# Kernel optimization log

Measured on AMD Instinct MI355X. Metric: run time of the kernel, lower is better.

## Reference

```python
import jax, jax.numpy as jnp
import numpy as np

B, T, DIM, DIM_EPS, H = 4, 1024, 2048, 2048, 16
HD = DIM // H        # 128, value head dim
HDE = DIM_EPS // H   # 128, q/k head dim


def setup_inputs() -> dict:
    key = jax.random.key(0)
    ks = jax.random.split(key, 6)
    s = 0.02
    # rotary frequencies as in llama-style precompute (theta=10000)
    inv_freq = 1.0 / (10000.0 ** (np.arange(0, HDE, 2, dtype=np.float32) / HDE))
    t = np.arange(T, dtype=np.float32)
    ang = np.outer(t, inv_freq)  # (T, HDE//2)
    return {
        "v": jax.random.normal(ks[0], (B, T, DIM), jnp.float32),
        "x_eps": jax.random.normal(ks[1], (B, T, DIM_EPS), jnp.float32),
        "freqs_cos": jnp.asarray(np.cos(ang)),
        "freqs_sin": jnp.asarray(np.sin(ang)),
        "W_eps_attn": jax.random.normal(ks[2], (DIM_EPS, 2 * DIM_EPS), jnp.float32) * s,
        "W_attn": jax.random.normal(ks[3], (DIM, DIM), jnp.float32) * s,
        "W_proj": jax.random.normal(ks[4], (DIM, DIM), jnp.float32) * s,
        "W_eps_proj": jax.random.normal(ks[5], (DIM_EPS, DIM_EPS), jnp.float32) * s,
    }


def _rope(x, cos, sin):
    # x: (B, T, H, HDE) -> complex-multiply by freqs_cis of shape (T, HDE//2)
    xr = x.reshape(*x.shape[:-1], -1, 2)
    x_re, x_im = xr[..., 0], xr[..., 1]
    c = cos[None, :, None, :]  # (1, T, 1, HDE//2)
    s = sin[None, :, None, :]
    o_re = x_re * c - x_im * s
    o_im = x_re * s + x_im * c
    return jnp.stack([o_re, o_im], axis=-1).reshape(x.shape)


def reference(v, x_eps, freqs_cos, freqs_sin, W_eps_attn, W_attn, W_proj, W_eps_proj):
    Bn, Tn, C = v.shape
    qk = x_eps @ W_eps_attn            # (B, T, 2*DIM_EPS)
    q, k = jnp.split(qk, 2, axis=-1)
    vp = v @ W_attn                    # (B, T, DIM)
    q = _rope(q.reshape(Bn, Tn, H, HDE), freqs_cos, freqs_sin)
    k = _rope(k.reshape(Bn, Tn, H, HDE), freqs_cos, freqs_sin)
    q = q.transpose(0, 2, 1, 3)        # (B, H, T, HDE)
    k = k.transpose(0, 2, 1, 3)
    vh = vp.reshape(Bn, Tn, H, HD).transpose(0, 2, 1, 3)
    scale = 1.0 / jnp.sqrt(jnp.asarray(HDE, q.dtype))
    scores = jnp.einsum("bhqd,bhkd->bhqk", q, k) * scale
    causal = jnp.tril(jnp.ones((Tn, Tn), bool))
    scores = jnp.where(causal[None, None], scores, jnp.finfo(scores.dtype).min)
    att = jax.nn.softmax(scores, axis=-1)
    y = jnp.einsum("bhqk,bhkd->bhqd", att, vh)
    y = y.transpose(0, 2, 1, 3).reshape(Bn, Tn, C)
    v_out = y @ W_proj
    x_eps_out = x_eps @ W_eps_proj
    return (v_out, x_eps_out)
```

## Files before the change

kernel.cpp:

```cpp
#include <hip/hip_runtime.h>
#include <stdint.h>

typedef __attribute__((ext_vector_type(8))) short  short8;
typedef __attribute__((ext_vector_type(4))) float  f32x4;
typedef __attribute__((ext_vector_type(4))) float  float4v;
typedef __attribute__((ext_vector_type(4))) unsigned short ushort4v;
typedef __attribute__((ext_vector_type(4))) unsigned int   u32x4;

#define DEV __device__ __forceinline__

DEV unsigned short f2bf(float f) {
    union { float f; unsigned int u; } x; x.f = f;
    unsigned int u = x.u;
    unsigned int r = (u + 0x7fffu + ((u >> 16) & 1u)) >> 16;
    return (unsigned short)r;
}
DEV float bf2f(unsigned short b) {
    union { unsigned int u; float f; } x; x.u = ((unsigned int)b) << 16;
    return x.f;
}

DEV void gll16(const void* g, void* l) {
    __builtin_amdgcn_global_load_lds(
        (const __attribute__((address_space(1))) void*)g,
        (__attribute__((address_space(3))) void*)l, 16, 0, 0);
}

#define MROWS 4096
#define KDIM  2048
#define NQK   4096

__global__ void prep_kernel(
    const float* __restrict__ xeps, const float* __restrict__ v_in,
    const float* __restrict__ Wea, const float* __restrict__ Wa,
    const float* __restrict__ Wp,  const float* __restrict__ Wep,
    unsigned short* __restrict__ xe16, unsigned short* __restrict__ v16,
    unsigned short* __restrict__ WeaT, unsigned short* __restrict__ WaT,
    unsigned short* __restrict__ WpT,  unsigned short* __restrict__ WepT) {

    __shared__ float tile[32][33];
    const int blk = blockIdx.x, tid = threadIdx.x;

    if (blk < 16384) {
        const float* in = (blk < 8192) ? xeps : v_in;
        unsigned short* out = (blk < 8192) ? xe16 : v16;
        int i = (blk & 8191) * 256 + tid;
        float4v f = ((const float4v*)in)[i];
        ushort4v o;
        o[0] = f2bf(f[0]); o[1] = f2bf(f[1]); o[2] = f2bf(f[2]); o[3] = f2bf(f[3]);
        ((ushort4v*)out)[i] = o;
        return;
    }
    const float* W; unsigned short* Wt; int K, N, local;
    if (blk < 24576)      { W = Wea; Wt = WeaT; K = KDIM; N = NQK;  local = blk - 16384; }
    else if (blk < 28672) { W = Wa;  Wt = WaT;  K = KDIM; N = KDIM; local = blk - 24576; }
    else if (blk < 32768) { W = Wp;  Wt = WpT;  K = KDIM; N = KDIM; local = blk - 28672; }
    else                  { W = Wep; Wt = WepT; K = KDIM; N = KDIM; local = blk - 32768; }
    const int ntiles = N >> 5;
    const int n0 = (local % ntiles) * 32, k0 = (local / ntiles) * 32;
    const int tx = tid & 31, ty = tid >> 5;
#pragma unroll
    for (int j = 0; j < 32; j += 8)
        tile[ty + j][tx] = W[(size_t)(k0 + ty + j) * N + n0 + tx];
    __syncthreads();
#pragma unroll
    for (int j = 0; j < 32; j += 8)
        Wt[(size_t)(n0 + ty + j) * K + k0 + tx] = f2bf(tile[tx][ty + j]);
}

__global__ void add_f32(float* __restrict__ out, const float* __restrict__ add, int n4) {
    int i = blockIdx.x * blockDim.x + threadIdx.x;
    if (i < n4) {
        float4v a = ((const float4v*)out)[i];
        float4v b = ((const float4v*)add)[i];
        a[0] += b[0]; a[1] += b[1]; a[2] += b[2]; a[3] += b[3];
        ((float4v*)out)[i] = a;
    }
}

__global__ void transpose_v(const unsigned short* __restrict__ vp,
                            unsigned short* __restrict__ vpT) {
    __shared__ unsigned short tile[32][34];
    int tx = threadIdx.x, ty = threadIdx.y;
    int R0 = blockIdx.y * 32;
    int c0 = blockIdx.x * 32;
    int bh = R0 >> 7, d0 = R0 & 127;
    int b = bh >> 4, h = bh & 15;
#pragma unroll
    for (int j = 0; j < 32; j += 8)
        tile[ty + j][tx] = vp[(size_t)(b * 1024 + c0 + ty + j) * 2048 + h * 128 + d0 + tx];
    __syncthreads();
#pragma unroll
    for (int j = 0; j < 32; j += 8)
        vpT[(size_t)(R0 + ty + j) * 1024 + c0 + tx] = tile[tx][ty + j];
}

__global__ __launch_bounds__(512, 2) void gemm256(
    const unsigned short* __restrict__ A0g, const unsigned short* __restrict__ B0g,
    float* __restrict__ Cf0, unsigned short* __restrict__ Ch0,
    int N0, int tx0, int nb0, int outbf0,
    const unsigned short* __restrict__ A1g, const unsigned short* __restrict__ B1g,
    float* __restrict__ Cf1, unsigned short* __restrict__ Ch1,
    int N1, int tx1, int outbf1, int Kst, int Kl,
    const float* __restrict__ rC, const float* __restrict__ rS,
    int rope0, int rope1) {

    __shared__ __align__(16) char lds[131072];

    int blk = blockIdx.x;
    const unsigned short* Ag; const unsigned short* Bg;
    float* Cf; unsigned short* Ch; int N, tx, outbf, nwg, ropeF;
    if (blk < nb0) { Ag = A0g; Bg = B0g; Cf = Cf0; Ch = Ch0; N = N0; tx = tx0; outbf = outbf0; nwg = nb0; ropeF = rope0; }
    else { blk -= nb0; Ag = A1g; Bg = B1g; Cf = Cf1; Ch = Ch1; N = N1; tx = tx1; outbf = outbf1; nwg = gridDim.x - nb0; ropeF = rope1; }
    { int cpx = nwg >> 3; blk = (blk & 7) * cpx + (blk >> 3); }
    const int bx = blk % tx, by = blk / tx;

    const int tid = threadIdx.x;
    const int lane = tid & 63;
    const int w  = tid >> 6;
    const int lr = lane & 15, lk = lane >> 4;
    const int wm = w >> 2, wn = w & 3;
    const int cswz16 = (lk ^ ((lr >> 3) << 1)) * 16;
    const int rdOff  = lr * 64 + cswz16;
    const int bRow0B = (wn & 1) * 4096;

    const unsigned short* Arow = Ag + (size_t)(by * 256) * Kst;
    const unsigned short* Brow = Bg + (size_t)(bx * 256) * Kst;

    const int srow = tid >> 2;
    const int sclog = (tid & 3) ^ (((tid >> 5) & 1) << 1);
    const unsigned short* aSt0 = Arow + (size_t)srow * Kst + sclog * 8;
    const unsigned short* aSt1 = aSt0 + (size_t)128 * Kst;
    const unsigned short* bSt0 = Brow + (size_t)srow * Kst + sclog * 8;
    const unsigned short* bSt1 = bSt0 + (size_t)128 * Kst;

    char* sA0 = lds;            char* sB0 = lds + 32768;
    char* sA1 = lds + 65536;    char* sB1 = lds + 98304;
    const int sOff = tid * 16;

    const char* aB0 = lds + wm * 16384;
    const char* aB1 = aB0 + 65536;
    const char* bB0 = lds + 32768 + (wn >> 1) * 16384;
    const char* bB1 = bB0 + 65536;

    f32x4 acc[8][4];
#pragma unroll
    for (int m = 0; m < 8; ++m)
#pragma unroll
        for (int n = 0; n < 4; ++n) acc[m][n] = (f32x4){0.f, 0.f, 0.f, 0.f};

    const int NT = Kl >> 6;

    auto STAGE = [&](const unsigned short* srcHalf, int k0, char* ldsHalf) {
        gll16(srcHalf + k0,      ldsHalf + sOff);
        gll16(srcHalf + k0 + 32, ldsHalf + 8192 + sOff);
    };

    STAGE(aSt0, 0, sA0);  STAGE(aSt1, 0, sA0 + 16384);
    STAGE(bSt0, 0, sB0);  STAGE(bSt1, 0, sB0 + 16384);
    STAGE(aSt0, 64, sA1);
    asm volatile("s_waitcnt vmcnt(2)" ::: "memory");
    __builtin_amdgcn_s_barrier();

#define MFMA_BF(a, b, c) __builtin_amdgcn_mfma_f32_16x16x32_bf16(a, b, c, 0, 0, 0)

#define RD_A(BASE, MH)                                                               \
    _Pragma("unroll") for (int i = 0; i < 4; ++i) {                                  \
        Ar[i][0] = *(const short8*)((BASE) +        (MH) * 4096 + i * 1024 + rdOff); \
        Ar[i][1] = *(const short8*)((BASE) + 8192 + (MH) * 4096 + i * 1024 + rdOff); \
    }

#define RD_B(BASE, NH)                                                                        \
    _Pragma("unroll") for (int j = 0; j < 2; ++j) {                                           \
        Br[j][0] = *(const short8*)((BASE) +        bRow0B + ((NH) * 2 + j) * 1024 + rdOff);  \
        Br[j][1] = *(const short8*)((BASE) + 8192 + bRow0B + ((NH) * 2 + j) * 1024 + rdOff);  \
    }

#define MFMA16(MH, NH)                                                       \
    __builtin_amdgcn_s_setprio(1);                                           \
    _Pragma("unroll") for (int ks = 0; ks < 2; ++ks)                         \
        _Pragma("unroll") for (int i = 0; i < 4; ++i)                        \
            _Pragma("unroll") for (int j = 0; j < 2; ++j)                    \
                acc[(MH) * 4 + i][(NH) * 2 + j] =                            \
                    MFMA_BF(Ar[i][ks], Br[j][ks], acc[(MH) * 4 + i][(NH) * 2 + j]); \
    __builtin_amdgcn_s_setprio(0);

#define PH(RDS, STG, MFMAQ, VMW)                               \
    {                                                          \
        RDS;                                                   \
        STG;                                                   \
        __builtin_amdgcn_s_barrier();                          \
        asm volatile("s_waitcnt lgkmcnt(0)" ::: "memory");     \
        __builtin_amdgcn_sched_barrier(0);                     \
        MFMAQ;                                                 \
        VMW;                                                   \
        __builtin_amdgcn_s_barrier();                          \
    }

#define VMC2 asm volatile("s_waitcnt vmcnt(2)" ::: "memory")

    short8 Ar[4][2], Br[2][2];

    for (int i2 = 0; i2 < NT; i2 += 2) {
        const int kt1 = (i2 + 1) * 64;
        const int kA  = (i2 + 2 < NT ? i2 + 2 : NT - 1) * 64;
        const int kA3 = (i2 + 3 < NT ? i2 + 3 : NT - 1) * 64;

        PH({ RD_A(aB0, 0) RD_B(bB0, 0) },
           { STAGE(aSt1, kt1, sA1 + 16384); STAGE(bSt0, kt1, sB1); STAGE(bSt1, kt1, sB1 + 16384); },
           MFMA16(0, 0), {})
        PH({ RD_B(bB0, 1) }, {}, MFMA16(0, 1), {})
        PH({ RD_A(aB0, 1) RD_B(bB0, 0) }, {}, MFMA16(1, 0), {})
        PH({ RD_B(bB0, 1) },
           { STAGE(aSt0, kA, sA0); },
           MFMA16(1, 1), VMC2)

        PH({ RD_A(aB1, 0) RD_B(bB1, 0) },
           { STAGE(aSt1, kA, sA0 + 16384); STAGE(bSt0, kA, sB0); STAGE(bSt1, kA, sB0 + 16384); },
           MFMA16(0, 0), {})
        PH({ RD_B(bB1, 1) }, {}, MFMA16(0, 1), {})
        PH({ RD_A(aB1, 1) RD_B(bB1, 0) }, {}, MFMA16(1, 0), {})
        PH({ RD_B(bB1, 1) },
           { STAGE(aSt0, kA3, sA1); },
           MFMA16(1, 1), VMC2)
    }
    asm volatile("s_waitcnt vmcnt(0)" ::: "memory");
#undef RD_A
#undef RD_B
#undef MFMA16
#undef PH
#undef VMC2

    if (outbf) {
        if (ropeF) {
#pragma unroll
            for (int mf = 0; mf < 8; ++mf)
#pragma unroll
                for (int nf = 0; nf < 4; ++nf)
#pragma unroll
                    for (int r = 0; r < 4; ++r) {
                        int row = by * 256 + wm * 128 + mf * 16 + lk * 4 + r;
                        int col = bx * 256 + wn * 64 + nf * 16 + lr;
                        float val = acc[mf][nf][r];
                        float part = __shfl_xor(val, 1);
                        int t = row & 1023;
                        int i = (col & 127) >> 1;
                        float c = rC[t * 64 + i];
                        float s = rS[t * 64 + i];
                        float o = (lr & 1) ? (part * s + val * c)
                                           : (val * c - part * s);
                        Ch[(size_t)row * N + col] = f2bf(o);
                    }
        } else {
#pragma unroll
            for (int mf = 0; mf < 8; ++mf)
#pragma unroll
                for (int nf = 0; nf < 4; ++nf)
#pragma unroll
                    for (int r = 0; r < 4; ++r) {
                        int row = by * 256 + wm * 128 + mf * 16 + lk * 4 + r;
                        int col = bx * 256 + wn * 64 + nf * 16 + lr;
                        Ch[(size_t)row * N + col] = f2bf(acc[mf][nf][r]);
                    }
        }
    } else {
#pragma unroll
        for (int mf = 0; mf < 8; ++mf)
#pragma unroll
            for (int nf = 0; nf < 4; ++nf)
#pragma unroll
                for (int r = 0; r < 4; ++r) {
                    int row = by * 256 + wm * 128 + mf * 16 + lk * 4 + r;
                    int col = bx * 256 + wn * 64 + nf * 16 + lr;
                    Cf[(size_t)row * N + col] = acc[mf][nf][r];
                }
    }
}

__global__ __launch_bounds__(256) void attn_kernel(
    const unsigned short* __restrict__ qk,
    const unsigned short* __restrict__ vpT,
    unsigned short* __restrict__ y) {

    const int bh = blockIdx.x;
    const int qt = 7 - (int)blockIdx.y;
    const int b = bh >> 4, h = bh & 15;
    const int qb0 = qt * 128;

    __shared__ __align__(16) unsigned short Kt[64 * 128];
    __shared__ __align__(16) unsigned short Vt[128 * 64];
    __shared__ __align__(16) unsigned short Pl[4 * 32 * 72];

    const int tid = threadIdx.x, w = tid >> 6, lane = tid & 63;
    const int lr = lane & 15, lk = lane >> 4;

    const unsigned short* Qb = qk + (size_t)(b * 1024) * 4096 + h * 128;
    const unsigned short* Kb = Qb + 2048;
    const unsigned short* Vg = vpT + (size_t)bh * 128 * 1024;
    unsigned short* Pw = &Pl[w * 32 * 72];


    short8 qf[2][4];
#pragma unroll
    for (int m = 0; m < 2; ++m) {
        const unsigned short* qrow = Qb + (size_t)(qb0 + w * 32 + m * 16 + lr) * 4096;
#pragma unroll
        for (int db = 0; db < 4; ++db)
            qf[m][db] = *(const short8*)(qrow + db * 32 + lk * 8);
    }

    f32x4 acc[2][8];
#pragma unroll
    for (int m = 0; m < 2; ++m)
#pragma unroll
        for (int n = 0; n < 8; ++n) acc[m][n] = (f32x4){0.f, 0.f, 0.f, 0.f};
    float m_i[2][4], l_i[2][4];
#pragma unroll
    for (int m = 0; m < 2; ++m)
#pragma unroll
        for (int r = 0; r < 4; ++r) { m_i[m][r] = -1e30f; l_i[m][r] = 0.f; }

    const int nkt = 2 * qt + 2;

#pragma unroll
    for (int c = 0; c < 4; ++c) {
        int base = w * 4096 + c * 1024;
        int row  = (base >> 8) + (lane >> 4);
        int scol = ((lane & 15) * 16) ^ ((row & 7) << 4);
        gll16(Kb + (size_t)row * 4096 + (scol >> 1), (char*)Kt + base);
        int d    = (base >> 7) + (lane >> 3);
        int svol = ((lane & 7) * 16) ^ ((d & 7) << 4);
        gll16(Vg + (size_t)d * 1024 + (svol >> 1), (char*)Vt + base);
    }
    __syncthreads();

    u32x4 kreg[4], vreg[4];

    for (int kt = 0; kt < nkt; ++kt) {
        const bool pf = (kt + 1 < nkt);
        if (pf) {
            const int ktn = kt + 1;
#pragma unroll
            for (int c = 0; c < 4; ++c) {
                int base = w * 4096 + c * 1024;
                int row  = (base >> 8) + (lane >> 4);
                int scol = ((lane & 15) * 16) ^ ((row & 7) << 4);
                kreg[c] = *(const u32x4*)(Kb + (size_t)(ktn * 64 + row) * 4096 + (scol >> 1));
                int d    = (base >> 7) + (lane >> 3);
                int svol = ((lane & 7) * 16) ^ ((d & 7) << 4);
                vreg[c] = *(const u32x4*)(Vg + (size_t)d * 1024 + ktn * 64 + (svol >> 1));
            }
        }

        f32x4 s[2][4];
#pragma unroll
        for (int m = 0; m < 2; ++m)
#pragma unroll
            for (int n = 0; n < 4; ++n) s[m][n] = (f32x4){0.f, 0.f, 0.f, 0.f};
#pragma unroll
        for (int db = 0; db < 4; ++db)
#pragma unroll
            for (int n = 0; n < 4; ++n) {
                int krow = n * 16 + lr;
                int cb = (db * 64 + lk * 16) ^ ((krow & 7) << 4);
                short8 kf = *(const short8*)((const char*)Kt + krow * 256 + cb);
                s[0][n] = __builtin_amdgcn_mfma_f32_16x16x32_bf16(qf[0][db], kf, s[0][n], 0, 0, 0);
                s[1][n] = __builtin_amdgcn_mfma_f32_16x16x32_bf16(qf[1][db], kf, s[1][n], 0, 0, 0);
            }

        const float sc = 0.08838834764831845f;
        const bool diag = (kt >= 2 * qt);
#pragma unroll
        for (int m = 0; m < 2; ++m)
#pragma unroll
            for (int n = 0; n < 4; ++n)
#pragma unroll
                for (int r = 0; r < 4; ++r) {
                    float v = s[m][n][r] * sc;
                    if (diag) {
                        int q   = qb0 + w * 32 + m * 16 + lk * 4 + r;
                        int key = kt * 64 + n * 16 + lr;
                        if (key > q) v = -1e30f;
                    }
                    s[m][n][r] = v;
                }

#pragma unroll
        for (int m = 0; m < 2; ++m) {
            float pm[4];
#pragma unroll
            for (int r = 0; r < 4; ++r)
                pm[r] = fmaxf(fmaxf(s[m][0][r], s[m][1][r]), fmaxf(s[m][2][r], s[m][3][r]));
#pragma unroll
            for (int o = 1; o < 16; o <<= 1)
#pragma unroll
                for (int r = 0; r < 4; ++r)
                    pm[r] = fmaxf(pm[r], __shfl_xor(pm[r], o, 16));

            bool small = true;
#pragma unroll
            for (int r = 0; r < 4; ++r)
                small = small && (pm[r] <= m_i[m][r] + 8.0f);
            if (!__all((int)small)) {
                float resc[4];
#pragma unroll
                for (int r = 0; r < 4; ++r) {
                    float mn = fmaxf(m_i[m][r], pm[r]);
                    resc[r] = __expf(m_i[m][r] - mn);
                    m_i[m][r] = mn;
                    l_i[m][r] *= resc[r];
                }
#pragma unroll
                for (int n = 0; n < 8; ++n)
#pragma unroll
                    for (int r = 0; r < 4; ++r)
                        acc[m][n][r] *= resc[r];
            }

            float rs[4] = {0.f, 0.f, 0.f, 0.f};
#pragma unroll
            for (int n = 0; n < 4; ++n)
#pragma unroll
                for (int r = 0; r < 4; ++r) {
                    float p = __expf(s[m][n][r] - m_i[m][r]);
                    s[m][n][r] = p;
                    rs[r] += p;
                }
#pragma unroll
            for (int o = 1; o < 16; o <<= 1)
#pragma unroll
                for (int r = 0; r < 4; ++r)
                    rs[r] += __shfl_xor(rs[r], o, 16);
#pragma unroll
            for (int r = 0; r < 4; ++r)
                l_i[m][r] += rs[r];

#pragma unroll
            for (int n = 0; n < 4; ++n)
#pragma unroll
                for (int r = 0; r < 4; ++r)
                    Pw[(m * 16 + lk * 4 + r) * 72 + n * 16 + lr] = f2bf(s[m][n][r]);
        }

#pragma unroll
        for (int ks = 0; ks < 2; ++ks) {
            short8 pf0 = *(const short8*)&Pw[(lr) * 72 + ks * 32 + lk * 8];
            short8 pf1 = *(const short8*)&Pw[(16 + lr) * 72 + ks * 32 + lk * 8];
#pragma unroll
            for (int n8 = 0; n8 < 8; ++n8) {
                int d  = n8 * 16 + lr;
                int cb = (ks * 64 + lk * 16) ^ ((d & 7) << 4);
                short8 vf = *(const short8*)((const char*)Vt + d * 128 + cb);
                acc[0][n8] = __builtin_amdgcn_mfma_f32_16x16x32_bf16(pf0, vf, acc[0][n8], 0, 0, 0);
                acc[1][n8] = __builtin_amdgcn_mfma_f32_16x16x32_bf16(pf1, vf, acc[1][n8], 0, 0, 0);
            }
        }
        __syncthreads();

        if (pf) {
#pragma unroll
            for (int c = 0; c < 4; ++c) {
                int base = w * 4096 + c * 1024;
                *(u32x4*)((char*)Kt + base + lane * 16) = kreg[c];
                *(u32x4*)((char*)Vt + base + lane * 16) = vreg[c];
            }
        }
        __syncthreads();
    }

    unsigned short* yb = y + (size_t)(b * 1024) * 2048 + h * 128;
#pragma unroll
    for (int m = 0; m < 2; ++m)
#pragma unroll
        for (int n8 = 0; n8 < 8; ++n8)
#pragma unroll
            for (int r = 0; r < 4; ++r) {
                int t = qb0 + w * 32 + m * 16 + lk * 4 + r;
                int d = n8 * 16 + lr;
                yb[(size_t)t * 2048 + d] = f2bf(acc[m][n8][r] / l_i[m][r]);
            }
}

extern "C" void kernel_launch(void* const* d_in, const int* in_sizes, int n_in,
                              void* d_out, int out_size, void* d_ws, size_t ws_size,
                              hipStream_t stream) {
    const float* v_in  = (const float*)d_in[0];
    const float* xeps  = (const float*)d_in[1];
    const float* fcos  = (const float*)d_in[2];
    const float* fsin  = (const float*)d_in[3];
    const float* Wea   = (const float*)d_in[4];
    const float* Wa    = (const float*)d_in[5];
    const float* Wp    = (const float*)d_in[6];
    const float* Wep   = (const float*)d_in[7];
    float* out = (float*)d_out;

    char* ws = (char*)d_ws;
    unsigned short* xe16 = (unsigned short*)ws;  ws += (size_t)MROWS * KDIM * 2;
    unsigned short* v16  = (unsigned short*)ws;  ws += (size_t)MROWS * KDIM * 2;
    unsigned short* WeaT = (unsigned short*)ws;  ws += (size_t)NQK * KDIM * 2;
    unsigned short* WaT  = (unsigned short*)ws;  ws += (size_t)KDIM * KDIM * 2;
    unsigned short* WpT  = (unsigned short*)ws;  ws += (size_t)KDIM * KDIM * 2;
    unsigned short* WepT = (unsigned short*)ws;  ws += (size_t)KDIM * KDIM * 2;
    unsigned short* qk16 = (unsigned short*)ws;  ws += (size_t)MROWS * NQK * 2;
    unsigned short* vp16 = (unsigned short*)ws;  ws += (size_t)MROWS * KDIM * 2;
    unsigned short* y16  = (unsigned short*)ws;  ws += (size_t)MROWS * KDIM * 2;
    unsigned short* vpT  = v16;
    float* projP = (float*)qk16;

    prep_kernel<<<36864, 256, 0, stream>>>(xeps, v_in, Wea, Wa, Wp, Wep,
                                           xe16, v16, WeaT, WaT, WpT, WepT);

    gemm256<<<256, 512, 0, stream>>>(
        xe16, WeaT, nullptr, qk16, NQK, 16, 256, 1,
        xe16, WeaT, nullptr, qk16, NQK, 16, 1, KDIM, KDIM,
        fcos, fsin, 1, 1);

    gemm256<<<256, 512, 0, stream>>>(
        v16,  WaT,  nullptr, vp16, KDIM, 8, 128, 1,
        xe16, WepT, out + (size_t)MROWS * KDIM, nullptr, KDIM, 8, 0, KDIM, KDIM,
        fcos, fsin, 0, 0);

    transpose_v<<<dim3(1024 / 32, 8192 / 32), dim3(32, 8), 0, stream>>>(vp16, vpT);

    attn_kernel<<<dim3(64, 8), 256, 0, stream>>>(qk16, vpT, y16);

    gemm256<<<256, 512, 0, stream>>>(
        y16,        WpT,        out,   nullptr, KDIM, 8, 128, 0,
        y16 + 1024, WpT + 1024, projP, nullptr, KDIM, 8, 0, KDIM, 1024,
        fcos, fsin, 0, 0);

    add_f32<<<8192, 256, 0, stream>>>(out, projP, MROWS * KDIM / 4);
}
```

Baseline: 306.3 us.

## Switch GEMM mainloop to 32x32x16 MFMA with new LDS layout and pipeline

```diff
diff --git a/kernel.cpp b/kernel.cpp
--- a/kernel.cpp
+++ b/kernel.cpp
@@ -1,11 +1,12 @@
 #include <hip/hip_runtime.h>
 #include <stdint.h>
 
-typedef __attribute__((ext_vector_type(8))) short  short8;
-typedef __attribute__((ext_vector_type(4))) float  f32x4;
-typedef __attribute__((ext_vector_type(4))) float  float4v;
-typedef __attribute__((ext_vector_type(4))) unsigned short ushort4v;
-typedef __attribute__((ext_vector_type(4))) unsigned int   u32x4;
+typedef __attribute__((ext_vector_type(8)))  short  short8;
+typedef __attribute__((ext_vector_type(4)))  float  f32x4;
+typedef __attribute__((ext_vector_type(16))) float  f32x16;
+typedef __attribute__((ext_vector_type(4)))  float  float4v;
+typedef __attribute__((ext_vector_type(4)))  unsigned short ushort4v;
+typedef __attribute__((ext_vector_type(4)))  unsigned int   u32x4;
 
 #define DEV __device__ __forceinline__
 
@@ -115,164 +116,151 @@
     { int cpx = nwg >> 3; blk = (blk & 7) * cpx + (blk >> 3); }
     const int bx = blk % tx, by = blk / tx;
 
-    const int tid = threadIdx.x;
+    const int tid  = threadIdx.x;
     const int lane = tid & 63;
-    const int w  = tid >> 6;
-    const int lr = lane & 15, lk = lane >> 4;
+    const int w    = tid >> 6;
     const int wm = w >> 2, wn = w & 3;
-    const int cswz16 = (lk ^ ((lr >> 3) << 1)) * 16;
-    const int rdOff  = lr * 64 + cswz16;
-    const int bRow0B = (wn & 1) * 4096;
+    const int l31 = lane & 31, hl = lane >> 5, l7 = lane & 7;
+
+    int co[4];
+#pragma unroll
+    for (int ks = 0; ks < 4; ++ks)
+        co[ks] = ((((ks << 1) | hl) ^ l7) << 4);
 
     const unsigned short* Arow = Ag + (size_t)(by * 256) * Kst;
     const unsigned short* Brow = Bg + (size_t)(bx * 256) * Kst;
 
-    const int srow = tid >> 2;
-    const int sclog = (tid & 3) ^ (((tid >> 5) & 1) << 1);
-    const unsigned short* aSt0 = Arow + (size_t)srow * Kst + sclog * 8;
-    const unsigned short* aSt1 = aSt0 + (size_t)128 * Kst;
-    const unsigned short* bSt0 = Brow + (size_t)srow * Kst + sclog * 8;
-    const unsigned short* bSt1 = bSt0 + (size_t)128 * Kst;
-
-    char* sA0 = lds;            char* sB0 = lds + 32768;
-    char* sA1 = lds + 65536;    char* sB1 = lds + 98304;
+    const int srw = tid >> 3;
+    const int sgc = (((tid & 7) ^ (srw & 7)) << 3);
+    const size_t r64 = (size_t)64 * Kst;
+    const unsigned short* aS = Arow + (size_t)srw * Kst + sgc;
+    const unsigned short* bS = Brow + (size_t)srw * Kst + sgc;
+
     const int sOff = tid * 16;
 
-    const char* aB0 = lds + wm * 16384;
-    const char* aB1 = aB0 + 65536;
-    const char* bB0 = lds + 32768 + (wn >> 1) * 16384;
-    const char* bB1 = bB0 + 65536;
-
-    f32x4 acc[8][4];
-#pragma unroll
-    for (int m = 0; m < 8; ++m)
-#pragma unroll
-        for (int n = 0; n < 4; ++n) acc[m][n] = (f32x4){0.f, 0.f, 0.f, 0.f};
+    const int aRB = (wm * 128 + l31) * 128;
+    const int bRB = (wn * 64  + l31) * 128;
+
+    f32x16 acc[4][2];
+#pragma unroll
+    for (int rt = 0; rt < 4; ++rt)
+#pragma unroll
+        for (int ct = 0; ct < 2; ++ct)
+#pragma unroll
+            for (int r = 0; r < 16; ++r) acc[rt][ct][r] = 0.f;
 
     const int NT = Kl >> 6;
 
-    auto STAGE = [&](const unsigned short* srcHalf, int k0, char* ldsHalf) {
-        gll16(srcHalf + k0,      ldsHalf + sOff);
-        gll16(srcHalf + k0 + 32, ldsHalf + 8192 + sOff);
+    auto STAGE4 = [&](const unsigned short* g, int k0, char* region) {
+#pragma unroll
+        for (int rb = 0; rb < 4; ++rb)
+            gll16(g + rb * r64 + k0, region + rb * 8192 + sOff);
     };
 
-    STAGE(aSt0, 0, sA0);  STAGE(aSt1, 0, sA0 + 16384);
-    STAGE(bSt0, 0, sB0);  STAGE(bSt1, 0, sB0 + 16384);
-    STAGE(aSt0, 64, sA1);
-    asm volatile("s_waitcnt vmcnt(2)" ::: "memory");
-    __builtin_amdgcn_s_barrier();
-
-#define MFMA_BF(a, b, c) __builtin_amdgcn_mfma_f32_16x16x32_bf16(a, b, c, 0, 0, 0)
-
-#define RD_A(BASE, MH)                                                               \
-    _Pragma("unroll") for (int i = 0; i < 4; ++i) {                                  \
-        Ar[i][0] = *(const short8*)((BASE) +        (MH) * 4096 + i * 1024 + rdOff); \
-        Ar[i][1] = *(const short8*)((BASE) + 8192 + (MH) * 4096 + i * 1024 + rdOff); \
-    }
-
-#define RD_B(BASE, NH)                                                                        \
-    _Pragma("unroll") for (int j = 0; j < 2; ++j) {                                           \
-        Br[j][0] = *(const short8*)((BASE) +        bRow0B + ((NH) * 2 + j) * 1024 + rdOff);  \
-        Br[j][1] = *(const short8*)((BASE) + 8192 + bRow0B + ((NH) * 2 + j) * 1024 + rdOff);  \
-    }
-
-#define MFMA16(MH, NH)                                                       \
-    __builtin_amdgcn_s_setprio(1);                                           \
-    _Pragma("unroll") for (int ks = 0; ks < 2; ++ks)                         \
-        _Pragma("unroll") for (int i = 0; i < 4; ++i)                        \
-            _Pragma("unroll") for (int j = 0; j < 2; ++j)                    \
-                acc[(MH) * 4 + i][(NH) * 2 + j] =                            \
-                    MFMA_BF(Ar[i][ks], Br[j][ks], acc[(MH) * 4 + i][(NH) * 2 + j]); \
-    __builtin_amdgcn_s_setprio(0);
-
-#define PH(RDS, STG, MFMAQ, VMW)                               \
-    {                                                          \
-        RDS;                                                   \
-        STG;                                                   \
-        __builtin_amdgcn_s_barrier();                          \
-        asm volatile("s_waitcnt lgkmcnt(0)" ::: "memory");     \
-        __builtin_amdgcn_sched_barrier(0);                     \
-        MFMAQ;                                                 \
-        VMW;                                                   \
-        __builtin_amdgcn_s_barrier();                          \
-    }
-
-#define VMC2 asm volatile("s_waitcnt vmcnt(2)" ::: "memory")
-
-    short8 Ar[4][2], Br[2][2];
-
-    for (int i2 = 0; i2 < NT; i2 += 2) {
-        const int kt1 = (i2 + 1) * 64;
-        const int kA  = (i2 + 2 < NT ? i2 + 2 : NT - 1) * 64;
-        const int kA3 = (i2 + 3 < NT ? i2 + 3 : NT - 1) * 64;
-
-        PH({ RD_A(aB0, 0) RD_B(bB0, 0) },
-           { STAGE(aSt1, kt1, sA1 + 16384); STAGE(bSt0, kt1, sB1); STAGE(bSt1, kt1, sB1 + 16384); },
-           MFMA16(0, 0), {})
-        PH({ RD_B(bB0, 1) }, {}, MFMA16(0, 1), {})
-        PH({ RD_A(aB0, 1) RD_B(bB0, 0) }, {}, MFMA16(1, 0), {})
-        PH({ RD_B(bB0, 1) },
-           { STAGE(aSt0, kA, sA0); },
-           MFMA16(1, 1), VMC2)
-
-        PH({ RD_A(aB1, 0) RD_B(bB1, 0) },
-           { STAGE(aSt1, kA, sA0 + 16384); STAGE(bSt0, kA, sB0); STAGE(bSt1, kA, sB0 + 16384); },
-           MFMA16(0, 0), {})
-        PH({ RD_B(bB1, 1) }, {}, MFMA16(0, 1), {})
-        PH({ RD_A(aB1, 1) RD_B(bB1, 0) }, {}, MFMA16(1, 0), {})
-        PH({ RD_B(bB1, 1) },
-           { STAGE(aSt0, kA3, sA1); },
-           MFMA16(1, 1), VMC2)
+#define MFMA32(a, b, c) __builtin_amdgcn_mfma_f32_32x32x16_bf16(a, b, c, 0, 0, 0)
+#define LGKM0 asm volatile("s_waitcnt lgkmcnt(0)" ::: "memory"); \
+              __builtin_amdgcn_sched_barrier(0)
+#define BARR  __builtin_amdgcn_s_barrier()
+
+    STAGE4(aS, 0,  lds);
+    STAGE4(bS, 0,  lds + 32768);
+    STAGE4(bS, 64, lds + 98304);
+    asm volatile("s_waitcnt vmcnt(4)" ::: "memory");
+    BARR;
+
+    short8 Af[2][4], Bf[2][4];
+
+    for (int t = 0; t < NT; ++t) {
+        const int par = t & 1;
+        const char* aC = lds + (par ? 65536 : 0);
+        const char* bC = lds + (par ? 98304 : 32768);
+        char* aN = lds + (par ? 0 : 65536);
+        char* bSame = lds + (par ? 98304 : 32768);
+        const int kA = (t + 1 < NT ? t + 1 : NT - 1) * 64;
+        const int kB = (t + 2 < NT ? t + 2 : NT - 1) * 64;
+
+#pragma unroll
+        for (int ct = 0; ct < 2; ++ct)
+#pragma unroll
+            for (int ks = 0; ks < 4; ++ks)
+                Bf[ct][ks] = *(const short8*)(bC + bRB + ct * 4096 + co[ks]);
+#pragma unroll
+        for (int j = 0; j < 2; ++j)
+#pragma unroll
+            for (int ks = 0; ks < 4; ++ks)
+                Af[j][ks] = *(const short8*)(aC + aRB + j * 4096 + co[ks]);
+        STAGE4(aS, kA, aN);
+        BARR;
+        LGKM0;
+        __builtin_amdgcn_s_setprio(1);
+#pragma unroll
+        for (int ks = 0; ks < 4; ++ks)
+#pragma unroll
+            for (int j = 0; j < 2; ++j)
+#pragma unroll
+                for (int ct = 0; ct < 2; ++ct)
+                    acc[j][ct] = MFMA32(Af[j][ks], Bf[ct][ks], acc[j][ct]);
+        __builtin_amdgcn_s_setprio(0);
+        BARR;
+
+#pragma unroll
+        for (int j = 0; j < 2; ++j)
+#pragma unroll
+            for (int ks = 0; ks < 4; ++ks)
+                Af[j][ks] = *(const short8*)(aC + aRB + (2 + j) * 4096 + co[ks]);
+        STAGE4(bS, kB, bSame);
+        BARR;
+        LGKM0;
+        __builtin_amdgcn_s_setprio(1);
+#pragma unroll
+        for (int ks = 0; ks < 4; ++ks)
+#pragma unroll
+            for (int j = 0; j < 2; ++j)
+#pragma unroll
+                for (int ct = 0; ct < 2; ++ct)
+                    acc[2 + j][ct] = MFMA32(Af[j][ks], Bf[ct][ks], acc[2 + j][ct]);
+        __builtin_amdgcn_s_setprio(0);
+        asm volatile("s_waitcnt vmcnt(4)" ::: "memory");
+        BARR;
     }
     asm volatile("s_waitcnt vmcnt(0)" ::: "memory");
-#undef RD_A
-#undef RD_B
-#undef MFMA16
-#undef PH
-#undef VMC2
-
+#undef MFMA32
+#undef LGKM0
+#undef BARR
+
+    const int colB = bx * 256 + wn * 64 + l31;
+    const int rowB = by * 256 + wm * 128 + 4 * hl;
     if (outbf) {
-        if (ropeF) {
-#pragma unroll
-            for (int mf = 0; mf < 8; ++mf)
-#pragma unroll
-                for (int nf = 0; nf < 4; ++nf)
-#pragma unroll
-                    for (int r = 0; r < 4; ++r) {
-                        int row = by * 256 + wm * 128 + mf * 16 + lk * 4 + r;
-                        int col = bx * 256 + wn * 64 + nf * 16 + lr;
-                        float val = acc[mf][nf][r];
+#pragma unroll
+        for (int rt = 0; rt < 4; ++rt)
+#pragma unroll
+            for (int ct = 0; ct < 2; ++ct)
+#pragma unroll
+                for (int reg = 0; reg < 16; ++reg) {
+                    int row = rowB + rt * 32 + (reg & 3) + 8 * (reg >> 2);
+                    int col = colB + ct * 32;
+                    float val = acc[rt][ct][reg];
+                    if (ropeF) {
                         float part = __shfl_xor(val, 1);
-                        int t = row & 1023;
-                        int i = (col & 127) >> 1;
-                        float c = rC[t * 64 + i];
-                        float s = rS[t * 64 + i];
-                        float o = (lr & 1) ? (part * s + val * c)
-                                           : (val * c - part * s);
-                        Ch[(size_t)row * N + col] = f2bf(o);
+                        int tt = row & 1023;
+                        int ii = (col & 127) >> 1;
+                        float c = rC[tt * 64 + ii];
+                        float s = rS[tt * 64 + ii];
+                        val = (l31 & 1) ? (part * s + val * c)
+                                        : (val * c - part * s);
                     }
-        } else {
-#pragma unroll
-            for (int mf = 0; mf < 8; ++mf)
-#pragma unroll
-                for (int nf = 0; nf < 4; ++nf)
-#pragma unroll
-                    for (int r = 0; r < 4; ++r) {
-                        int row = by * 256 + wm * 128 + mf * 16 + lk * 4 + r;
-                        int col = bx * 256 + wn * 64 + nf * 16 + lr;
-                        Ch[(size_t)row * N + col] = f2bf(acc[mf][nf][r]);
-                    }
-        }
+                    Ch[(size_t)row * N + col] = f2bf(val);
+                }
     } else {
 #pragma unroll
-        for (int mf = 0; mf < 8; ++mf)
-#pragma unroll
-            for (int nf = 0; nf < 4; ++nf)
-#pragma unroll
-                for (int r = 0; r < 4; ++r) {
-                    int row = by * 256 + wm * 128 + mf * 16 + lk * 4 + r;
-                    int col = bx * 256 + wn * 64 + nf * 16 + lr;
-                    Cf[(size_t)row * N + col] = acc[mf][nf][r];
+        for (int rt = 0; rt < 4; ++rt)
+#pragma unroll
+            for (int ct = 0; ct < 2; ++ct)
+#pragma unroll
+                for (int reg = 0; reg < 16; ++reg) {
+                    int row = rowB + rt * 32 + (reg & 3) + 8 * (reg >> 2);
+                    int col = colB + ct * 32;
+                    Cf[(size_t)row * N + col] = acc[rt][ct][reg];
                 }
     }
 }
@@ -298,7 +286,6 @@
     const unsigned short* Kb = Qb + 2048;
     const unsigned short* Vg = vpT + (size_t)bh * 128 * 1024;
     unsigned short* Pw = &Pl[w * 32 * 72];
-
 
     short8 qf[2][4];
 #pragma unroll
```

After: 339.3 us. 10.8% more time.
